# Kernel tuning notes

Measured on AMD Instinct MI355X. Metric: run time of the kernel, lower is better.

Reference implementation:

```python
import jax, jax.numpy as jnp
import numpy as np

E = 8        # n_routed_experts
Z = 4        # zero_expert_num (identity experts)
K = 2        # moe_topk
SCALE = 2.5  # routed_scaling_factor
T, H, I = 8192, 1024, 512


def setup_inputs() -> dict:
    key = jax.random.key(0)
    k0, k1, k2, k3, k4 = jax.random.split(key, 5)
    return {
        "hidden_states": jax.random.normal(k0, (T, H), jnp.float32),
        "router_w": jax.random.normal(k1, (E + Z, H), jnp.float32) * 0.02,
        "correction_bias": jax.random.normal(k2, (E + Z,), jnp.float32) * 0.01,
        "w13": jax.random.normal(k3, (E, 2 * I, H), jnp.float32) * 0.02,
        "w2": jax.random.normal(k4, (E, H, I), jnp.float32) * 0.02,
    }


def reference(hidden_states, router_w, correction_bias, w13, w2):
    # ---- router (float32) ----
    logits = hidden_states.astype(jnp.float32) @ router_w.T          # [T, E+Z]
    scores = jax.nn.softmax(logits, axis=-1)
    # correction bias only affects expert *selection*, not the gate weights
    _, topk_idx = jax.lax.top_k(scores + correction_bias, K)          # [T, K]
    topk_w = jnp.take_along_axis(scores, topk_idx, axis=-1)          # renormalize=False

    # ---- zero experts (identity type): idx >= E contributes scale * x ----
    is_zero = topk_idx >= E                                           # [T, K]
    routed_w = jnp.where(is_zero, 0.0, topk_w)
    zero_scale = jnp.where(is_zero, topk_w, 0.0).sum(-1, keepdims=True)
    zero_result = zero_scale * hidden_states                          # [T, H]

    # ---- combine weights per routed expert: [T, E] ----
    tok = jnp.arange(hidden_states.shape[0])[:, None]
    safe_idx = jnp.clip(topk_idx, 0, E - 1)   # zero-expert slots carry weight 0
    combine = jnp.zeros((hidden_states.shape[0], E), scores.dtype)
    combine = combine.at[tok, safe_idx].add(routed_w)

    # ---- grouped expert GEMMs (SiLU gated MLP), combined densely ----
    h = jnp.einsum('th,eih->eti', hidden_states, w13)                 # [E, T, 2I]
    g, u = jnp.split(h, 2, axis=-1)
    act = jax.nn.silu(g) * u                                          # [E, T, I]
    eo = jnp.einsum('eti,ehi->eth', act, w2)                          # [E, T, H]
    routed = jnp.einsum('te,eth->th', combine, eo)                    # [T, H]

    return routed * SCALE + zero_result
```

## Files before the change

kernel.cpp:

```cpp
#include <hip/hip_runtime.h>
#include <hip/hip_bf16.h>
#include <math.h>

typedef __bf16 bf16_t;
typedef bf16_t bf16x4 __attribute__((ext_vector_type(4)));
typedef bf16_t bf16x8 __attribute__((ext_vector_type(8)));
typedef float f32x4 __attribute__((ext_vector_type(4)));

#define T_TOK 8192
#define HDIM  1024
#define IDIM  512
#define NEXP  8
#define NTOT  12
#define MAXROWS (2 * T_TOK + NEXP * 128)
#define MAX_MTILES (MAXROWS / 128)

__device__ __forceinline__ void gll16(const bf16_t* g, bf16_t* l) {
  __builtin_amdgcn_global_load_lds((__attribute__((address_space(1))) void*)g,
                                   (__attribute__((address_space(3))) void*)l,
                                   16, 0, 0);
}

__global__ void wcast_init_kernel(const float* __restrict__ w13, const float* __restrict__ w2,
                                  bf16_t* __restrict__ w13b, bf16_t* __restrict__ w2b,
                                  int* __restrict__ sel_tok, float* __restrict__ sel_w) {
  size_t gid = (size_t)blockIdx.x * blockDim.x + threadIdx.x;
  if (gid < MAXROWS) { sel_tok[gid] = 0; sel_w[gid] = 0.f; }
  const size_t n13 = (size_t)NEXP * 2 * IDIM * HDIM / 8;
  const size_t n2  = (size_t)NEXP * HDIM * IDIM / 8;
  const float* in; bf16_t* out; size_t i;
  if (gid < n13)            { in = w13; out = w13b; i = gid * 8; }
  else if (gid < n13 + n2)  { in = w2;  out = w2b;  i = (gid - n13) * 8; }
  else return;
  float4 a = *(const float4*)&in[i];
  float4 b = *(const float4*)&in[i + 4];
  bf16x8 o;
  o[0] = (bf16_t)a.x; o[1] = (bf16_t)a.y; o[2] = (bf16_t)a.z; o[3] = (bf16_t)a.w;
  o[4] = (bf16_t)b.x; o[5] = (bf16_t)b.y; o[6] = (bf16_t)b.z; o[7] = (bf16_t)b.w;
  *(bf16x8*)&out[i] = o;
}

__global__ void router_kernel(const float* __restrict__ x, const float* __restrict__ rw,
                              const float* __restrict__ bias,
                              int* __restrict__ tk_e, float* __restrict__ tk_w,
                              float* __restrict__ zscale, bf16_t* __restrict__ xb) {
  int t = blockIdx.x;
  int l = threadIdx.x;
  const float4* xr = (const float4*)(x + (size_t)t * HDIM);
  float4 xv[4];
#pragma unroll
  for (int i = 0; i < 4; i++) xv[i] = xr[l + 64 * i];
#pragma unroll
  for (int i = 0; i < 4; i++) {
    bf16x4 o;
    o[0] = (bf16_t)xv[i].x; o[1] = (bf16_t)xv[i].y;
    o[2] = (bf16_t)xv[i].z; o[3] = (bf16_t)xv[i].w;
    *(bf16x4*)&xb[(size_t)t * HDIM + (size_t)(l + 64 * i) * 4] = o;
  }
  float part[NTOT];
#pragma unroll
  for (int e = 0; e < NTOT; e++) {
    const float4* wr = (const float4*)(rw + (size_t)e * HDIM);
    float s = 0.f;
#pragma unroll
    for (int i = 0; i < 4; i++) {
      float4 w = wr[l + 64 * i];
      s += xv[i].x * w.x + xv[i].y * w.y + xv[i].z * w.z + xv[i].w * w.w;
    }
    part[e] = s;
  }
#pragma unroll
  for (int off = 32; off > 0; off >>= 1)
#pragma unroll
    for (int e = 0; e < NTOT; e++) part[e] += __shfl_down(part[e], off);

  if (l == 0) {
    float mx = part[0];
#pragma unroll
    for (int e = 1; e < NTOT; e++) mx = fmaxf(mx, part[e]);
    float p[NTOT], den = 0.f;
#pragma unroll
    for (int e = 0; e < NTOT; e++) { p[e] = expf(part[e] - mx); den += p[e]; }
    float inv = 1.f / den;
#pragma unroll
    for (int e = 0; e < NTOT; e++) p[e] *= inv;
    float s0 = -1e30f, s1 = -1e30f; int i0 = 0, i1 = 0;
#pragma unroll
    for (int e = 0; e < NTOT; e++) {
      float v = p[e] + bias[e];
      if (v > s0) { s1 = s0; i1 = i0; s0 = v; i0 = e; }
      else if (v > s1) { s1 = v; i1 = e; }
    }
    float zs = 0.f;
    int idx[2] = { i0, i1 };
#pragma unroll
    for (int k = 0; k < 2; k++) {
      int e = idx[k];
      float w = p[e];
      if (e >= NEXP) { zs += w; tk_e[2 * t + k] = -1; tk_w[2 * t + k] = 0.f; }
      else           { tk_e[2 * t + k] = e; tk_w[2 * t + k] = w; }
    }
    zscale[t] = zs;
  }
}

__global__ void countscan_kernel(const int* __restrict__ tk_e, int* __restrict__ cursor,
                                 int* __restrict__ total_rows, int* __restrict__ tile_e,
                                 int* __restrict__ tile_p0, int* __restrict__ n_mtiles) {
  __shared__ int lc[NEXP];
  int tid = threadIdx.x;
  if (tid < NEXP) lc[tid] = 0;
  __syncthreads();
  int cnt[NEXP];
#pragma unroll
  for (int j = 0; j < NEXP; j++) cnt[j] = 0;
  for (int i = tid; i < 2 * T_TOK; i += 256) {
    int e = tk_e[i];
#pragma unroll
    for (int j = 0; j < NEXP; j++) cnt[j] += (e == j) ? 1 : 0;
  }
#pragma unroll
  for (int off = 32; off > 0; off >>= 1)
#pragma unroll
    for (int j = 0; j < NEXP; j++) cnt[j] += __shfl_down(cnt[j], off);
  if ((tid & 63) == 0)
#pragma unroll
    for (int j = 0; j < NEXP; j++) atomicAdd(&lc[j], cnt[j]);
  __syncthreads();
  if (tid == 0) {
    int run = 0, nt = 0;
    for (int e = 0; e < NEXP; e++) {
      cursor[e] = run;
      int ntile = (lc[e] + 127) / 128;
      for (int i = 0; i < ntile; i++) {
        tile_e[nt] = e;
        tile_p0[nt] = run + i * 128;
        nt++;
      }
      run += ntile * 128;
    }
    *total_rows = run;
    *n_mtiles = nt;
  }
}

__global__ void assign_kernel(const int* __restrict__ tk_e, const float* __restrict__ tk_w,
                              int* __restrict__ cursor, int* __restrict__ sel_tok,
                              float* __restrict__ sel_w, int* __restrict__ pos) {
  __shared__ int lc[NEXP];
  __shared__ int lbase[NEXP];
  int tid = threadIdx.x;
  if (tid < NEXP) lc[tid] = 0;
  __syncthreads();
  int t = blockIdx.x * blockDim.x + tid;
  int e0 = tk_e[2 * t], e1 = tk_e[2 * t + 1];
  int r0 = (e0 >= 0) ? atomicAdd(&lc[e0], 1) : -1;
  int r1 = (e1 >= 0) ? atomicAdd(&lc[e1], 1) : -1;
  __syncthreads();
  if (tid < NEXP) lbase[tid] = atomicAdd(&cursor[tid], lc[tid]);
  __syncthreads();
  int p0 = -1, p1 = -1;
  if (e0 >= 0) { p0 = lbase[e0] + r0; sel_tok[p0] = t; sel_w[p0] = 2.5f * tk_w[2 * t]; }
  if (e1 >= 0) { p1 = lbase[e1] + r1; sel_tok[p1] = t; sel_w[p1] = 2.5f * tk_w[2 * t + 1]; }
  pos[2 * t] = p0;
  pos[2 * t + 1] = p1;
}

__global__ __launch_bounds__(256) void gemm1_kernel(
    const bf16_t* __restrict__ xb, const bf16_t* __restrict__ w13b,
    const int* __restrict__ sel_tok, const int* __restrict__ tile_e,
    const int* __restrict__ tile_p0, const int* __restrict__ n_mtiles,
    bf16_t* __restrict__ actb) {
  const int ti = blockIdx.x;
  if (ti >= *n_mtiles) return;
  const int e = tile_e[ti];
  const int p0 = tile_p0[ti];
  const int g0 = blockIdx.y * 64;

  __shared__ alignas(16) bf16_t As[128 * 64];
  __shared__ alignas(16) bf16_t Bs[128 * 64];
  const int tid = threadIdx.x;
  const int w = tid >> 6, l = tid & 63;
  const int wr = w >> 1, wc = w & 1;
  const int quad = l >> 4, c16 = l & 15;

  const int lr = l >> 3;
  const int csrc = ((l & 7) ^ lr) * 8;
  const bf16_t* w13e = w13b + (size_t)e * (2 * IDIM) * HDIM;
  const bf16_t* Asrc[4];
  const bf16_t* Bsrc[4];
#pragma unroll
  for (int s = 0; s < 4; s++) {
    int r = w * 32 + s * 8 + lr;
    int tok = sel_tok[p0 + r];
    Asrc[s] = xb + (size_t)tok * HDIM + csrc;
    int col = g0 + (r >> 6) * 32 + (((r >> 4) & 1) * 16) + (r & 15) + (((r >> 5) & 1) ? IDIM : 0);
    Bsrc[s] = w13e + (size_t)col * HDIM + csrc;
  }
  bf16_t* Adst = &As[(w * 32) * 64];
  bf16_t* Bdst = &Bs[(w * 32) * 64];

  f32x4 acc[4][4];
#pragma unroll
  for (int i = 0; i < 4; i++)
#pragma unroll
    for (int j = 0; j < 4; j++) acc[i][j] = (f32x4){0.f, 0.f, 0.f, 0.f};

  for (int k0 = 0; k0 < HDIM; k0 += 64) {
#pragma unroll
    for (int s = 0; s < 4; s++) {
      gll16(Asrc[s] + k0, Adst + s * 8 * 64);
      gll16(Bsrc[s] + k0, Bdst + s * 8 * 64);
    }
    __syncthreads();
#pragma unroll
    for (int kk = 0; kk < 2; kk++) {
      bf16x8 af[4], bfv[4];
#pragma unroll
      for (int mt = 0; mt < 4; mt++)
        af[mt] = *(const bf16x8*)&As[(wr * 64 + mt * 16 + c16) * 64 + (((kk * 4 + quad) ^ (c16 & 7)) * 8)];
#pragma unroll
      for (int nt = 0; nt < 4; nt++)
        bfv[nt] = *(const bf16x8*)&Bs[(wc * 64 + nt * 16 + c16) * 64 + (((kk * 4 + quad) ^ (c16 & 7)) * 8)];
#pragma unroll
      for (int mt = 0; mt < 4; mt++)
#pragma unroll
        for (int nt = 0; nt < 4; nt++)
          acc[mt][nt] = __builtin_amdgcn_mfma_f32_16x16x32_bf16(af[mt], bfv[nt], acc[mt][nt], 0, 0, 0);
    }
    __syncthreads();
  }

#pragma unroll
  for (int mt = 0; mt < 4; mt++) {
    int rowb = p0 + wr * 64 + mt * 16 + quad * 4;
#pragma unroll
    for (int nt = 0; nt < 2; nt++) {
      int col = g0 + wc * 32 + nt * 16 + c16;
#pragma unroll
      for (int r = 0; r < 4; r++) {
        float g = acc[mt][nt][r];
        float u = acc[mt][nt + 2][r];
        float s = g / (1.f + expf(-g));
        actb[(size_t)(rowb + r) * IDIM + col] = (bf16_t)(s * u);
      }
    }
  }
}

__global__ __launch_bounds__(256) void gemm2_kernel(
    const bf16_t* __restrict__ actb, const bf16_t* __restrict__ w2b,
    const float* __restrict__ sel_w, const int* __restrict__ tile_e,
    const int* __restrict__ tile_p0, const int* __restrict__ n_mtiles,
    bf16_t* __restrict__ eob) {
  const int ti = blockIdx.x;
  if (ti >= *n_mtiles) return;
  const int e = tile_e[ti];
  const int p0 = tile_p0[ti];
  const int n0 = blockIdx.y * 128;

  __shared__ alignas(16) bf16_t As[128 * 64];
  __shared__ alignas(16) bf16_t Bs[128 * 64];
  const int tid = threadIdx.x;
  const int w = tid >> 6, l = tid & 63;
  const int wr = w >> 1, wc = w & 1;
  const int quad = l >> 4, c16 = l & 15;

  const int lr = l >> 3;
  const int csrc = ((l & 7) ^ lr) * 8;
  const bf16_t* Asrc[4];
  const bf16_t* Bsrc[4];
#pragma unroll
  for (int s = 0; s < 4; s++) {
    int r = w * 32 + s * 8 + lr;
    Asrc[s] = actb + (size_t)(p0 + r) * IDIM + csrc;
    Bsrc[s] = w2b + (size_t)e * HDIM * IDIM + (size_t)(n0 + r) * IDIM + csrc;
  }
  bf16_t* Adst = &As[(w * 32) * 64];
  bf16_t* Bdst = &Bs[(w * 32) * 64];

  f32x4 acc[4][4];
#pragma unroll
  for (int i = 0; i < 4; i++)
#pragma unroll
    for (int j = 0; j < 4; j++) acc[i][j] = (f32x4){0.f, 0.f, 0.f, 0.f};

  for (int k0 = 0; k0 < IDIM; k0 += 64) {
#pragma unroll
    for (int s = 0; s < 4; s++) {
      gll16(Asrc[s] + k0, Adst + s * 8 * 64);
      gll16(Bsrc[s] + k0, Bdst + s * 8 * 64);
    }
    __syncthreads();
#pragma unroll
    for (int kk = 0; kk < 2; kk++) {
      bf16x8 af[4], bfv[4];
#pragma unroll
      for (int mt = 0; mt < 4; mt++)
        af[mt] = *(const bf16x8*)&As[(wr * 64 + mt * 16 + c16) * 64 + (((kk * 4 + quad) ^ (c16 & 7)) * 8)];
#pragma unroll
      for (int nt = 0; nt < 4; nt++)
        bfv[nt] = *(const bf16x8*)&Bs[(wc * 64 + nt * 16 + c16) * 64 + (((kk * 4 + quad) ^ (c16 & 7)) * 8)];
#pragma unroll
      for (int mt = 0; mt < 4; mt++)
#pragma unroll
        for (int nt = 0; nt < 4; nt++)
          acc[mt][nt] = __builtin_amdgcn_mfma_f32_16x16x32_bf16(af[mt], bfv[nt], acc[mt][nt], 0, 0, 0);
    }
    __syncthreads();
  }

#pragma unroll
  for (int mt = 0; mt < 4; mt++) {
    int rowb = wr * 64 + mt * 16 + quad * 4;
    float cw[4];
#pragma unroll
    for (int r = 0; r < 4; r++) cw[r] = sel_w[p0 + rowb + r];
#pragma unroll
    for (int nt = 0; nt < 4; nt++) {
      int col = n0 + wc * 64 + nt * 16 + c16;
#pragma unroll
      for (int r = 0; r < 4; r++)
        eob[(size_t)(p0 + rowb + r) * HDIM + col] = (bf16_t)(cw[r] * acc[mt][nt][r]);
    }
  }
}

__global__ void combine_kernel(const float* __restrict__ x, const float* __restrict__ zscale,
                               const int* __restrict__ pos, const bf16_t* __restrict__ eob,
                               float* __restrict__ out) {
  size_t gid = (size_t)blockIdx.x * blockDim.x + threadIdx.x;
  size_t t = gid >> 7;
  size_t j = (gid & 127) << 3;
  float zs = zscale[t];
  int p0 = pos[2 * t], p1 = pos[2 * t + 1];
  float4 a = *(const float4*)&x[t * HDIM + j];
  float4 b = *(const float4*)&x[t * HDIM + j + 4];
  float o[8] = { zs * a.x, zs * a.y, zs * a.z, zs * a.w,
                 zs * b.x, zs * b.y, zs * b.z, zs * b.w };
  if (p0 >= 0) {
    bf16x8 v = *(const bf16x8*)&eob[(size_t)p0 * HDIM + j];
#pragma unroll
    for (int k = 0; k < 8; k++) o[k] += (float)v[k];
  }
  if (p1 >= 0) {
    bf16x8 v = *(const bf16x8*)&eob[(size_t)p1 * HDIM + j];
#pragma unroll
    for (int k = 0; k < 8; k++) o[k] += (float)v[k];
  }
  *(float4*)&out[t * HDIM + j] = make_float4(o[0], o[1], o[2], o[3]);
  *(float4*)&out[t * HDIM + j + 4] = make_float4(o[4], o[5], o[6], o[7]);
}

extern "C" void kernel_launch(void* const* d_in, const int* in_sizes, int n_in,
                              void* d_out, int out_size, void* d_ws, size_t ws_size,
                              hipStream_t stream) {
  const float* x    = (const float*)d_in[0];
  const float* rw   = (const float*)d_in[1];
  const float* bias = (const float*)d_in[2];
  const float* w13  = (const float*)d_in[3];
  const float* w2   = (const float*)d_in[4];
  float* out = (float*)d_out;

  char* ws = (char*)d_ws;
  bf16_t* w13b = (bf16_t*)ws;  ws += (size_t)NEXP * 2 * IDIM * HDIM * 2;
  bf16_t* w2b  = (bf16_t*)ws;  ws += (size_t)NEXP * HDIM * IDIM * 2;
  bf16_t* xb   = (bf16_t*)ws;  ws += (size_t)T_TOK * HDIM * 2;
  bf16_t* actb = (bf16_t*)ws;  ws += (size_t)MAXROWS * IDIM * 2;
  bf16_t* eob  = (bf16_t*)ws;  ws += (size_t)MAXROWS * HDIM * 2;
  int*   tk_e    = (int*)ws;   ws += (size_t)T_TOK * 2 * 4;
  float* tk_w    = (float*)ws; ws += (size_t)T_TOK * 2 * 4;
  float* zscale  = (float*)ws; ws += (size_t)T_TOK * 4;
  int*   pos     = (int*)ws;   ws += (size_t)T_TOK * 2 * 4;
  int*   sel_tok = (int*)ws;   ws += (size_t)MAXROWS * 4;
  float* sel_w   = (float*)ws; ws += (size_t)MAXROWS * 4;
  int*   cursor  = (int*)ws;   ws += NEXP * 4;
  int*   total_rows = (int*)ws; ws += 4;
  int*   tile_e  = (int*)ws;   ws += MAX_MTILES * 4;
  int*   tile_p0 = (int*)ws;   ws += MAX_MTILES * 4;
  int*   n_mtiles = (int*)ws;  ws += 4;

  {
    size_t n8 = (size_t)NEXP * 2 * IDIM * HDIM / 8 + (size_t)NEXP * HDIM * IDIM / 8;
    wcast_init_kernel<<<(n8 + 255) / 256, 256, 0, stream>>>(w13, w2, w13b, w2b,
                                                            sel_tok, sel_w);
  }
  router_kernel<<<T_TOK, 64, 0, stream>>>(x, rw, bias, tk_e, tk_w, zscale, xb);
  countscan_kernel<<<1, 256, 0, stream>>>(tk_e, cursor, total_rows,
                                          tile_e, tile_p0, n_mtiles);
  assign_kernel<<<T_TOK / 256, 256, 0, stream>>>(tk_e, tk_w, cursor, sel_tok, sel_w, pos);

  gemm1_kernel<<<dim3(MAX_MTILES, IDIM / 64), 256, 0, stream>>>(
      xb, w13b, sel_tok, tile_e, tile_p0, n_mtiles, actb);
  gemm2_kernel<<<dim3(MAX_MTILES, HDIM / 128), 256, 0, stream>>>(
      actb, w2b, sel_w, tile_e, tile_p0, n_mtiles, eob);

  combine_kernel<<<(size_t)T_TOK * HDIM / 8 / 256, 256, 0, stream>>>(
      x, zscale, pos, eob, out);
}
```

Baseline: 247.3 us.

## Fuse combine into gemm2 via atomic scatter and widen GEMM N tiles

```diff
diff --git a/kernel.cpp b/kernel.cpp
--- a/kernel.cpp
+++ b/kernel.cpp
@@ -43,7 +43,7 @@
 __global__ void router_kernel(const float* __restrict__ x, const float* __restrict__ rw,
                               const float* __restrict__ bias,
                               int* __restrict__ tk_e, float* __restrict__ tk_w,
-                              float* __restrict__ zscale, bf16_t* __restrict__ xb) {
+                              bf16_t* __restrict__ xb, float* __restrict__ out) {
   int t = blockIdx.x;
   int l = threadIdx.x;
   const float4* xr = (const float4*)(x + (size_t)t * HDIM);
@@ -74,6 +74,7 @@
 #pragma unroll
     for (int e = 0; e < NTOT; e++) part[e] += __shfl_down(part[e], off);
 
+  float zs = 0.f;
   if (l == 0) {
     float mx = part[0];
 #pragma unroll
@@ -91,7 +92,6 @@
       if (v > s0) { s1 = s0; i1 = i0; s0 = v; i0 = e; }
       else if (v > s1) { s1 = v; i1 = e; }
     }
-    float zs = 0.f;
     int idx[2] = { i0, i1 };
 #pragma unroll
     for (int k = 0; k < 2; k++) {
@@ -100,7 +100,12 @@
       if (e >= NEXP) { zs += w; tk_e[2 * t + k] = -1; tk_w[2 * t + k] = 0.f; }
       else           { tk_e[2 * t + k] = e; tk_w[2 * t + k] = w; }
     }
-    zscale[t] = zs;
+  }
+  zs = __shfl(zs, 0);
+#pragma unroll
+  for (int i = 0; i < 4; i++) {
+    float4 o = make_float4(zs * xv[i].x, zs * xv[i].y, zs * xv[i].z, zs * xv[i].w);
+    *(float4*)&out[(size_t)t * HDIM + (size_t)(l + 64 * i) * 4] = o;
   }
 }
 
@@ -146,7 +151,7 @@
 
 __global__ void assign_kernel(const int* __restrict__ tk_e, const float* __restrict__ tk_w,
                               int* __restrict__ cursor, int* __restrict__ sel_tok,
-                              float* __restrict__ sel_w, int* __restrict__ pos) {
+                              float* __restrict__ sel_w) {
   __shared__ int lc[NEXP];
   __shared__ int lbase[NEXP];
   int tid = threadIdx.x;
@@ -159,14 +164,11 @@
   __syncthreads();
   if (tid < NEXP) lbase[tid] = atomicAdd(&cursor[tid], lc[tid]);
   __syncthreads();
-  int p0 = -1, p1 = -1;
-  if (e0 >= 0) { p0 = lbase[e0] + r0; sel_tok[p0] = t; sel_w[p0] = 2.5f * tk_w[2 * t]; }
-  if (e1 >= 0) { p1 = lbase[e1] + r1; sel_tok[p1] = t; sel_w[p1] = 2.5f * tk_w[2 * t + 1]; }
-  pos[2 * t] = p0;
-  pos[2 * t + 1] = p1;
-}
-
-__global__ __launch_bounds__(256) void gemm1_kernel(
+  if (e0 >= 0) { int p = lbase[e0] + r0; sel_tok[p] = t; sel_w[p] = 2.5f * tk_w[2 * t]; }
+  if (e1 >= 0) { int p = lbase[e1] + r1; sel_tok[p] = t; sel_w[p] = 2.5f * tk_w[2 * t + 1]; }
+}
+
+__global__ __launch_bounds__(256, 2) void gemm1_kernel(
     const bf16_t* __restrict__ xb, const bf16_t* __restrict__ w13b,
     const int* __restrict__ sel_tok, const int* __restrict__ tile_e,
     const int* __restrict__ tile_p0, const int* __restrict__ n_mtiles,
@@ -175,57 +177,57 @@
   if (ti >= *n_mtiles) return;
   const int e = tile_e[ti];
   const int p0 = tile_p0[ti];
-  const int g0 = blockIdx.y * 64;
+  const int g0 = blockIdx.y * 128;
 
   __shared__ alignas(16) bf16_t As[128 * 64];
-  __shared__ alignas(16) bf16_t Bs[128 * 64];
+  __shared__ alignas(16) bf16_t Bs[256 * 64];
   const int tid = threadIdx.x;
   const int w = tid >> 6, l = tid & 63;
   const int wr = w >> 1, wc = w & 1;
   const int quad = l >> 4, c16 = l & 15;
 
-  const int lr = l >> 3;
-  const int csrc = ((l & 7) ^ lr) * 8;
+  const int srow = tid >> 3;
+  const int csrc = ((tid & 7) ^ (srow & 7)) * 8;
   const bf16_t* w13e = w13b + (size_t)e * (2 * IDIM) * HDIM;
   const bf16_t* Asrc[4];
-  const bf16_t* Bsrc[4];
+  const bf16_t* Bsrc[8];
 #pragma unroll
   for (int s = 0; s < 4; s++) {
-    int r = w * 32 + s * 8 + lr;
-    int tok = sel_tok[p0 + r];
+    int tok = sel_tok[p0 + s * 32 + srow];
     Asrc[s] = xb + (size_t)tok * HDIM + csrc;
-    int col = g0 + (r >> 6) * 32 + (((r >> 4) & 1) * 16) + (r & 15) + (((r >> 5) & 1) ? IDIM : 0);
+  }
+#pragma unroll
+  for (int s = 0; s < 8; s++) {
+    int col = g0 + (s >> 1) * 32 + srow + ((s & 1) ? IDIM : 0);
     Bsrc[s] = w13e + (size_t)col * HDIM + csrc;
   }
-  bf16_t* Adst = &As[(w * 32) * 64];
-  bf16_t* Bdst = &Bs[(w * 32) * 64];
-
-  f32x4 acc[4][4];
+
+  f32x4 acc[4][8];
 #pragma unroll
   for (int i = 0; i < 4; i++)
 #pragma unroll
-    for (int j = 0; j < 4; j++) acc[i][j] = (f32x4){0.f, 0.f, 0.f, 0.f};
+    for (int j = 0; j < 8; j++) acc[i][j] = (f32x4){0.f, 0.f, 0.f, 0.f};
 
   for (int k0 = 0; k0 < HDIM; k0 += 64) {
 #pragma unroll
-    for (int s = 0; s < 4; s++) {
-      gll16(Asrc[s] + k0, Adst + s * 8 * 64);
-      gll16(Bsrc[s] + k0, Bdst + s * 8 * 64);
-    }
+    for (int s = 0; s < 4; s++) gll16(Asrc[s] + k0, &As[s * 2048 + w * 512]);
+#pragma unroll
+    for (int s = 0; s < 8; s++) gll16(Bsrc[s] + k0, &Bs[s * 2048 + w * 512]);
     __syncthreads();
 #pragma unroll
     for (int kk = 0; kk < 2; kk++) {
-      bf16x8 af[4], bfv[4];
+      const int kch = ((kk * 4 + quad) ^ (c16 & 7)) * 8;
+      bf16x8 af[4], bfv[8];
 #pragma unroll
       for (int mt = 0; mt < 4; mt++)
-        af[mt] = *(const bf16x8*)&As[(wr * 64 + mt * 16 + c16) * 64 + (((kk * 4 + quad) ^ (c16 & 7)) * 8)];
-#pragma unroll
-      for (int nt = 0; nt < 4; nt++)
-        bfv[nt] = *(const bf16x8*)&Bs[(wc * 64 + nt * 16 + c16) * 64 + (((kk * 4 + quad) ^ (c16 & 7)) * 8)];
+        af[mt] = *(const bf16x8*)&As[(wr * 64 + mt * 16 + c16) * 64 + kch];
+#pragma unroll
+      for (int nt = 0; nt < 8; nt++)
+        bfv[nt] = *(const bf16x8*)&Bs[(wc * 128 + nt * 16 + c16) * 64 + kch];
 #pragma unroll
       for (int mt = 0; mt < 4; mt++)
 #pragma unroll
-        for (int nt = 0; nt < 4; nt++)
+        for (int nt = 0; nt < 8; nt++)
           acc[mt][nt] = __builtin_amdgcn_mfma_f32_16x16x32_bf16(af[mt], bfv[nt], acc[mt][nt], 0, 0, 0);
     }
     __syncthreads();
@@ -235,8 +237,9 @@
   for (int mt = 0; mt < 4; mt++) {
     int rowb = p0 + wr * 64 + mt * 16 + quad * 4;
 #pragma unroll
-    for (int nt = 0; nt < 2; nt++) {
-      int col = g0 + wc * 32 + nt * 16 + c16;
+    for (int ntg = 0; ntg < 4; ntg++) {
+      int nt = (ntg & 1) + (ntg >> 1) * 4;
+      int col = g0 + (wc * 2 + (nt >> 2)) * 32 + (nt & 1) * 16 + c16;
 #pragma unroll
       for (int r = 0; r < 4; r++) {
         float g = acc[mt][nt][r];
@@ -248,63 +251,62 @@
   }
 }
 
-__global__ __launch_bounds__(256) void gemm2_kernel(
+__global__ __launch_bounds__(256, 2) void gemm2_kernel(
     const bf16_t* __restrict__ actb, const bf16_t* __restrict__ w2b,
-    const float* __restrict__ sel_w, const int* __restrict__ tile_e,
-    const int* __restrict__ tile_p0, const int* __restrict__ n_mtiles,
-    bf16_t* __restrict__ eob) {
+    const float* __restrict__ sel_w, const int* __restrict__ sel_tok,
+    const int* __restrict__ tile_e, const int* __restrict__ tile_p0,
+    const int* __restrict__ n_mtiles, float* __restrict__ out) {
   const int ti = blockIdx.x;
   if (ti >= *n_mtiles) return;
   const int e = tile_e[ti];
   const int p0 = tile_p0[ti];
-  const int n0 = blockIdx.y * 128;
+  const int n0 = blockIdx.y * 256;
 
   __shared__ alignas(16) bf16_t As[128 * 64];
-  __shared__ alignas(16) bf16_t Bs[128 * 64];
+  __shared__ alignas(16) bf16_t Bs[256 * 64];
   const int tid = threadIdx.x;
   const int w = tid >> 6, l = tid & 63;
   const int wr = w >> 1, wc = w & 1;
   const int quad = l >> 4, c16 = l & 15;
 
-  const int lr = l >> 3;
-  const int csrc = ((l & 7) ^ lr) * 8;
+  const int srow = tid >> 3;
+  const int csrc = ((tid & 7) ^ (srow & 7)) * 8;
+  const bf16_t* w2e = w2b + (size_t)e * HDIM * IDIM;
   const bf16_t* Asrc[4];
-  const bf16_t* Bsrc[4];
-#pragma unroll
-  for (int s = 0; s < 4; s++) {
-    int r = w * 32 + s * 8 + lr;
-    Asrc[s] = actb + (size_t)(p0 + r) * IDIM + csrc;
-    Bsrc[s] = w2b + (size_t)e * HDIM * IDIM + (size_t)(n0 + r) * IDIM + csrc;
-  }
-  bf16_t* Adst = &As[(w * 32) * 64];
-  bf16_t* Bdst = &Bs[(w * 32) * 64];
-
-  f32x4 acc[4][4];
+  const bf16_t* Bsrc[8];
+#pragma unroll
+  for (int s = 0; s < 4; s++)
+    Asrc[s] = actb + (size_t)(p0 + s * 32 + srow) * IDIM + csrc;
+#pragma unroll
+  for (int s = 0; s < 8; s++)
+    Bsrc[s] = w2e + (size_t)(n0 + s * 32 + srow) * IDIM + csrc;
+
+  f32x4 acc[4][8];
 #pragma unroll
   for (int i = 0; i < 4; i++)
 #pragma unroll
-    for (int j = 0; j < 4; j++) acc[i][j] = (f32x4){0.f, 0.f, 0.f, 0.f};
+    for (int j = 0; j < 8; j++) acc[i][j] = (f32x4){0.f, 0.f, 0.f, 0.f};
 
   for (int k0 = 0; k0 < IDIM; k0 += 64) {
 #pragma unroll
-    for (int s = 0; s < 4; s++) {
-      gll16(Asrc[s] + k0, Adst + s * 8 * 64);
-      gll16(Bsrc[s] + k0, Bdst + s * 8 * 64);
-    }
+    for (int s = 0; s < 4; s++) gll16(Asrc[s] + k0, &As[s * 2048 + w * 512]);
+#pragma unroll
+    for (int s = 0; s < 8; s++) gll16(Bsrc[s] + k0, &Bs[s * 2048 + w * 512]);
     __syncthreads();
 #pragma unroll
     for (int kk = 0; kk < 2; kk++) {
-      bf16x8 af[4], bfv[4];
+      const int kch = ((kk * 4 + quad) ^ (c16 & 7)) * 8;
+      bf16x8 af[4], bfv[8];
 #pragma unroll
       for (int mt = 0; mt < 4; mt++)
-        af[mt] = *(const bf16x8*)&As[(wr * 64 + mt * 16 + c16) * 64 + (((kk * 4 + quad) ^ (c16 & 7)) * 8)];
-#pragma unroll
-      for (int nt = 0; nt < 4; nt++)
-        bfv[nt] = *(const bf16x8*)&Bs[(wc * 64 + nt * 16 + c16) * 64 + (((kk * 4 + quad) ^ (c16 & 7)) * 8)];
+        af[mt] = *(const bf16x8*)&As[(wr * 64 + mt * 16 + c16) * 64 + kch];
+#pragma unroll
+      for (int nt = 0; nt < 8; nt++)
+        bfv[nt] = *(const bf16x8*)&Bs[(wc * 128 + nt * 16 + c16) * 64 + kch];
 #pragma unroll
       for (int mt = 0; mt < 4; mt++)
 #pragma unroll
-        for (int nt = 0; nt < 4; nt++)
+        for (int nt = 0; nt < 8; nt++)
           acc[mt][nt] = __builtin_amdgcn_mfma_f32_16x16x32_bf16(af[mt], bfv[nt], acc[mt][nt], 0, 0, 0);
     }
     __syncthreads();
@@ -312,44 +314,20 @@
 
 #pragma unroll
   for (int mt = 0; mt < 4; mt++) {
-    int rowb = wr * 64 + mt * 16 + quad * 4;
-    float cw[4];
-#pragma unroll
-    for (int r = 0; r < 4; r++) cw[r] = sel_w[p0 + rowb + r];
-#pragma unroll
-    for (int nt = 0; nt < 4; nt++) {
-      int col = n0 + wc * 64 + nt * 16 + c16;
-#pragma unroll
-      for (int r = 0; r < 4; r++)
-        eob[(size_t)(p0 + rowb + r) * HDIM + col] = (bf16_t)(cw[r] * acc[mt][nt][r]);
-    }
-  }
-}
-
-__global__ void combine_kernel(const float* __restrict__ x, const float* __restrict__ zscale,
-                               const int* __restrict__ pos, const bf16_t* __restrict__ eob,
-                               float* __restrict__ out) {
-  size_t gid = (size_t)blockIdx.x * blockDim.x + threadIdx.x;
-  size_t t = gid >> 7;
-  size_t j = (gid & 127) << 3;
-  float zs = zscale[t];
-  int p0 = pos[2 * t], p1 = pos[2 * t + 1];
-  float4 a = *(const float4*)&x[t * HDIM + j];
-  float4 b = *(const float4*)&x[t * HDIM + j + 4];
-  float o[8] = { zs * a.x, zs * a.y, zs * a.z, zs * a.w,
-                 zs * b.x, zs * b.y, zs * b.z, zs * b.w };
-  if (p0 >= 0) {
-    bf16x8 v = *(const bf16x8*)&eob[(size_t)p0 * HDIM + j];
-#pragma unroll
-    for (int k = 0; k < 8; k++) o[k] += (float)v[k];
-  }
-  if (p1 >= 0) {
-    bf16x8 v = *(const bf16x8*)&eob[(size_t)p1 * HDIM + j];
-#pragma unroll
-    for (int k = 0; k < 8; k++) o[k] += (float)v[k];
-  }
-  *(float4*)&out[t * HDIM + j] = make_float4(o[0], o[1], o[2], o[3]);
-  *(float4*)&out[t * HDIM + j + 4] = make_float4(o[4], o[5], o[6], o[7]);
+    int rowb = p0 + wr * 64 + mt * 16 + quad * 4;
+#pragma unroll
+    for (int r = 0; r < 4; r++) {
+      float cw = sel_w[rowb + r];
+      if (cw == 0.f) continue;
+      int tok = sel_tok[rowb + r];
+      float* orow = out + (size_t)tok * HDIM;
+#pragma unroll
+      for (int nt = 0; nt < 8; nt++) {
+        int col = n0 + wc * 128 + nt * 16 + c16;
+        atomicAdd(&orow[col], cw * acc[mt][nt][r]);
+      }
+    }
+  }
 }
 
 extern "C" void kernel_launch(void* const* d_in, const int* in_sizes, int n_in,
@@ -367,11 +345,8 @@
   bf16_t* w2b  = (bf16_t*)ws;  ws += (size_t)NEXP * HDIM * IDIM * 2;
   bf16_t* xb   = (bf16_t*)ws;  ws += (size_t)T_TOK * HDIM * 2;
   bf16_t* actb = (bf16_t*)ws;  ws += (size_t)MAXROWS * IDIM * 2;
-  bf16_t* eob  = (bf16_t*)ws;  ws += (size_t)MAXROWS * HDIM * 2;
   int*   tk_e    = (int*)ws;   ws += (size_t)T_TOK * 2 * 4;
   float* tk_w    = (float*)ws; ws += (size_t)T_TOK * 2 * 4;
-  float* zscale  = (float*)ws; ws += (size_t)T_TOK * 4;
-  int*   pos     = (int*)ws;   ws += (size_t)T_TOK * 2 * 4;
   int*   sel_tok = (int*)ws;   ws += (size_t)MAXROWS * 4;
   float* sel_w   = (float*)ws; ws += (size_t)MAXROWS * 4;
   int*   cursor  = (int*)ws;   ws += NEXP * 4;
@@ -385,16 +360,13 @@
     wcast_init_kernel<<<(n8 + 255) / 256, 256, 0, stream>>>(w13, w2, w13b, w2b,
                                                             sel_tok, sel_w);
   }
-  router_kernel<<<T_TOK, 64, 0, stream>>>(x, rw, bias, tk_e, tk_w, zscale, xb);
+  router_kernel<<<T_TOK, 64, 0, stream>>>(x, rw, bias, tk_e, tk_w, xb, out);
   countscan_kernel<<<1, 256, 0, stream>>>(tk_e, cursor, total_rows,
                                           tile_e, tile_p0, n_mtiles);
-  assign_kernel<<<T_TOK / 256, 256, 0, stream>>>(tk_e, tk_w, cursor, sel_tok, sel_w, pos);
-
-  gemm1_kernel<<<dim3(MAX_MTILES, IDIM / 64), 256, 0, stream>>>(
+  assign_kernel<<<T_TOK / 256, 256, 0, stream>>>(tk_e, tk_w, cursor, sel_tok, sel_w);
+
+  gemm1_kernel<<<dim3(MAX_MTILES, (2 * IDIM) / 256), 256, 0, stream>>>(
       xb, w13b, sel_tok, tile_e, tile_p0, n_mtiles, actb);
-  gemm2_kernel<<<dim3(MAX_MTILES, HDIM / 128), 256, 0, stream>>>(
-      actb, w2b, sel_w, tile_e, tile_p0, n_mtiles, eob);
-
-  combine_kernel<<<(size_t)T_TOK * HDIM / 8 / 256, 256, 0, stream>>>(
-      x, zscale, pos, eob, out);
-}
+  gemm2_kernel<<<dim3(MAX_MTILES, HDIM / 256), 256, 0, stream>>>(
+      actb, w2b, sel_w, sel_tok, tile_e, tile_p0, n_mtiles, out);
+}
```

Result: slower. 255.7 us (+3.4%).
